# Optimization experiments

Measured on AMD Instinct MI355X. Metric: run time of the kernel, lower is better.

## Reference

```python
import jax, jax.numpy as jnp
import numpy as np

B, T, N, F = 8, 24, 207, 16
H = 64            # hidden_dim
DH = 16           # dims_hyper[-1] / node-embedding out
DA = 4 * F        # temporal attention dim_out
DS = 64           # ss_gal gcn out dim (last_ss_gal_dim)
GDEP = 2
ALPHA, BETA, GAMMA = 0.05, 0.95, 0.95
TA = 2.0


def _lin(x, w, b=None):
    y = x @ w
    return y if b is None else y + b


def gcn_hyper(x, A, W, b):
    # x: [B,N,C], A: [N,N] static. h <- a*x + g * einsum('nvc,vw->nwc', h, A)
    h = x
    outs = [h]
    for _ in range(GDEP):
        h = ALPHA * x + GAMMA * jnp.einsum('bvc,vw->bwc', h, A)
        outs.append(h)
    return _lin(jnp.concatenate(outs, axis=-1), W, b)


def gcn_gru(x, A_dyn, A_sta, W, b):
    # x: [B,N,C], A_dyn: [B,N,N], A_sta: [N,N]
    h = x
    outs = [h]
    for _ in range(GDEP):
        h = (ALPHA * x
             + BETA * jnp.einsum('bvw,bvc->bwc', A_dyn, h)     # bmm(A^T, h)
             + GAMMA * jnp.einsum('bvc,vw->bwc', h, A_sta))
        outs.append(h)
    return _lin(jnp.concatenate(outs, axis=-1), W, b)


def gcn_ssgal(x, A, W, b):
    # x: [B*,N,C], A: [B*,N,N]
    h = x
    outs = [h]
    for _ in range(GDEP):
        h = ALPHA * x + GAMMA * jnp.einsum('bvw,bvc->bwc', A, h)
        outs.append(h)
    return _lin(jnp.concatenate(outs, axis=-1), W, b)


def setup_inputs() -> dict:
    key = jax.random.key(0)
    ks = jax.random.split(key, 32)
    i = iter(range(32))
    w = lambda *s: (0.02 * jax.random.normal(ks[next(i)], s, dtype=jnp.float32))
    inp = {
        'input_sequence': jax.random.normal(ks[next(i)], (B, T, N, F), dtype=jnp.float32),
        'static_adj': jax.random.uniform(ks[next(i)], (N, N), dtype=jnp.float32),
        # hyper graph generators: mlp in = (GDEP+1)*H -> DH
        'src_gen_w': w((GDEP + 1) * H, DH), 'src_gen_b': w(DH),
        'tgt_gen_w': w((GDEP + 1) * H, DH), 'tgt_gen_b': w(DH),
        # node embeddings: F -> DH
        'src_emb_w': w(F, DH), 'src_emb_b': w(DH),
        'tgt_emb_w': w(F, DH), 'tgt_emb_b': w(DH),
        # GRU gate GCNs: mlp in = (GDEP+1)*(F+H) -> H
        'gru_z_w': w((GDEP + 1) * (F + H), H), 'gru_z_b': w(H),
        'gru_r_w': w((GDEP + 1) * (F + H), H), 'gru_r_b': w(H),
        'gru_c_w': w((GDEP + 1) * (F + H), H), 'gru_c_b': w(H),
        # temporal attention: F -> DA, score DA -> 1
        'attn_q_w': w(F, DA),
        'attn_k_w': w(F, DA), 'attn_k_b': w(DA),
        'attn_s_w': w(DA, 1),
        # ss_gal spatial gcn: (GDEP+1)*F -> DS
        'sgcn_w': w((GDEP + 1) * F, DS), 'sgcn_b': w(DS),
        # predictors
        'short_w': w(DS, F), 'short_b': w(F),
        'long_w': w(H, F), 'long_b': w(F),
        'fus_w': w(DS + H, F), 'fus_b': w(F),
    }
    return inp


def _forward(input_sequence, static_adj,
             src_gen_w, src_gen_b, tgt_gen_w, tgt_gen_b,
             src_emb_w, src_emb_b, tgt_emb_w, tgt_emb_b,
             gru_z_w, gru_z_b, gru_r_w, gru_r_b, gru_c_w, gru_c_b,
             attn_q_w, attn_k_w, attn_k_b, attn_s_w,
             sgcn_w, sgcn_b,
             short_w, short_b, long_w, long_b, fus_w, fus_b):
    batch, steps, nodes = input_sequence.shape[0], input_sequence.shape[1], input_sequence.shape[2]
    eye = jnp.eye(nodes, dtype=input_sequence.dtype)

    def cell(x_t, h):
        # x_t: [B,N,F], h: [B,N,H]
        src_ctx = gcn_hyper(h, static_adj, src_gen_w, src_gen_b)   # [B,N,DH]
        tgt_ctx = gcn_hyper(h, static_adj, tgt_gen_w, tgt_gen_b)
        s = jnp.tanh(TA * _lin(x_t, src_emb_w, src_emb_b) * src_ctx)
        t = jnp.tanh(TA * _lin(x_t, tgt_emb_w, tgt_emb_b) * tgt_ctx)
        asym = jnp.einsum('bnc,bmc->bnm', s, t) - jnp.einsum('bnc,bmc->bnm', t, s)
        adj = jax.nn.relu(jnp.tanh(TA * asym)) + eye
        adj = adj / (adj.sum(axis=-1, keepdims=True) + 1e-8)
        gi = jnp.concatenate([x_t, h], axis=-1)
        z = jax.nn.sigmoid(gcn_gru(gi, adj, static_adj, gru_z_w, gru_z_b))
        r = jax.nn.sigmoid(gcn_gru(gi, adj, static_adj, gru_r_w, gru_r_b))
        ri = jnp.concatenate([x_t, r * h], axis=-1)
        c = jnp.tanh(gcn_gru(ri, adj, static_adj, gru_c_w, gru_c_b))
        return z * h + (1.0 - z) * c

    h = jnp.zeros((batch, nodes, H), dtype=input_sequence.dtype)
    for t_step in range(0, max(1, steps - 4), 4):
        h = cell(input_sequence[:, t_step], h)

    # ss_gal branch on the last 4 steps
    recent = input_sequence[:, -4:]            # [B,4,N,F]
    target = input_sequence[:, -1]             # [B,N,F]
    # temporal attention
    q = target @ attn_q_w                      # [B,N,DA]
    k = recent @ attn_k_w + attn_k_b           # [B,4,N,DA]
    scores = jnp.tanh(q[:, None, :, None, :] + k[:, :, None, :, :])  # [B,4,N,N,DA]
    scores = jnp.squeeze(scores @ attn_s_w, axis=-1)                  # [B,4,N,N]
    attn = jax.nn.softmax(scores, axis=-1)
    dyn_adj = static_adj[None] + attn.reshape(-1, nodes, nodes)       # [B*4,N,N]
    rh = recent.reshape(-1, nodes, recent.shape[-1])                  # [B*4,N,F]
    rh = gcn_ssgal(rh, dyn_adj, sgcn_w, sgcn_b)                       # [B*4,N,DS]
    rh = jax.nn.relu(rh.reshape(batch, -1, nodes, rh.shape[-1]))      # [B,4,N,DS]
    target = jnp.sum(rh, axis=1)                                       # [B,N,DS]

    short = _lin(target, short_w, short_b)      # [B,N,F]
    h = cell(short, h)                          # final GRU step on short-term prediction
    long = _lin(h, long_w, long_b)              # [B,N,F]
    fused = _lin(jnp.concatenate([target, h], axis=-1), fus_w, fus_b)  # [B,N,F]
    return jnp.stack([short, long, fused], axis=0)  # [3,B,N,F]


def reference(input_sequence, static_adj,
              src_gen_w, src_gen_b, tgt_gen_w, tgt_gen_b,
              src_emb_w, src_emb_b, tgt_emb_w, tgt_emb_b,
              gru_z_w, gru_z_b, gru_r_w, gru_r_b, gru_c_w, gru_c_b,
              attn_q_w, attn_k_w, attn_k_b, attn_s_w,
              sgcn_w, sgcn_b,
              short_w, short_b, long_w, long_b, fus_w, fus_b):
    return _forward(input_sequence, static_adj,
                    src_gen_w, src_gen_b, tgt_gen_w, tgt_gen_b,
                    src_emb_w, src_emb_b, tgt_emb_w, tgt_emb_b,
                    gru_z_w, gru_z_b, gru_r_w, gru_r_b, gru_c_w, gru_c_b,
                    attn_q_w, attn_k_w, attn_k_b, attn_s_w,
                    sgcn_w, sgcn_b,
                    short_w, short_b, long_w, long_b, fus_w, fus_b)
```

## Files before the change

kernel.cpp:

```cpp
#include <hip/hip_runtime.h>


constexpr int B = 8, T = 24, N = 207, F = 16, H = 64, DH = 16;
constexpr int PS = 208;
constexpr float ALPHA = 0.05f, BETA = 0.95f, GAMMA = 0.95f, TA = 2.0f;
constexpr int NF = N * F;
constexpr int BNF = B * N * F;

__device__ __forceinline__ float tanh_fast(float x) { float e = __expf(2.f * x); return 1.f - 2.f / (e + 1.f); }
__device__ __forceinline__ float sigm(float x) { return 1.f / (1.f + __expf(-x)); }
__device__ __forceinline__ float tanh_pnc(float x) {
    float x2 = x * x;
    float p = x * (27.f + x2);
    float q = 27.f + 9.f * x2;
    return p * __builtin_amdgcn_rcpf(q);
}

__global__ __launch_bounds__(256) void k_build_Ts(const float* __restrict__ adj, float* __restrict__ Ts) {
    int i = blockIdx.x * 256 + threadIdx.x;
    if (i >= N * N) return;
    int w = i / N, v = i % N;
    Ts[(size_t)w * PS + v] = adj[v * N + w];
}

__global__ __launch_bounds__(256) void k_mm_sq(const float* __restrict__ Ain, float* __restrict__ Aout) {
    const float* A = Ain;
    float* O = Aout;
    int w0 = blockIdx.x * 32, v0b = blockIdx.y * 32;
    int tid = threadIdx.x;
    __shared__ float sA[2][32][33], sB[2][32][33];
    float acc[4] = {0, 0, 0, 0};
    int i0 = tid >> 5, j = tid & 31;
    int r = tid >> 3, c4 = (tid & 7) * 4;
    float4 av, bv;
    auto loadT = [&](int u0) {
        av = make_float4(0, 0, 0, 0); bv = make_float4(0, 0, 0, 0);
        int w = w0 + r, u = u0 + r;
        if (w < N) av = *(const float4*)&A[(size_t)w * PS + u0 + c4];
        if (u < N) bv = *(const float4*)&A[(size_t)u * PS + v0b + c4];
    };
    loadT(0);
    int cur = 0;
    for (int t = 0; t < 7; t++) {
        __syncthreads();
        sA[cur][r][c4] = av.x; sA[cur][r][c4 + 1] = av.y; sA[cur][r][c4 + 2] = av.z; sA[cur][r][c4 + 3] = av.w;
        sB[cur][r][c4] = bv.x; sB[cur][r][c4 + 1] = bv.y; sB[cur][r][c4 + 2] = bv.z; sB[cur][r][c4 + 3] = bv.w;
        if (t < 6) loadT((t + 1) * 32);
        __syncthreads();
#pragma unroll 8
        for (int u_ = 0; u_ < 32; u_++) {
            float bvv = sB[cur][u_][j];
#pragma unroll
            for (int k = 0; k < 4; k++) acc[k] += sA[cur][i0 + k * 8][u_] * bvv;
        }
        cur ^= 1;
    }
#pragma unroll
    for (int k = 0; k < 4; k++) {
        int w = w0 + i0 + k * 8, v = v0b + j;
        if (w < N && v < N) O[(size_t)w * PS + v] = acc[k];
    }
}

__global__ __launch_bounds__(256) void k_cell_a(
    const float* __restrict__ h, const float* __restrict__ Ts, const float* __restrict__ A2,
    const float* __restrict__ xseq, int tsel, const float* __restrict__ xbuf,
    const float* __restrict__ Wsrc, const float* __restrict__ bsrc,
    const float* __restrict__ Wtgt, const float* __restrict__ btgt,
    const float* __restrict__ Wes, const float* __restrict__ bes,
    const float* __restrict__ Wet, const float* __restrict__ bet,
    float* __restrict__ s_out, float* __restrict__ t_out, float* __restrict__ catg) {
    int b = blockIdx.y, w0 = blockIdx.x * 16, lane = blockIdx.z;
    int tid = threadIdx.x, ty = tid >> 4, tx = tid & 15;
    __shared__ float sTs[2][16][33], sA2[2][16][33];
    __shared__ float sH[2][32][64];
    __shared__ float cat[16][193];
    __shared__ float sW[192][16];
    __shared__ float sX[16][16], sWe[16][16];
    float au[4] = {0, 0, 0, 0}, aw[4] = {0, 0, 0, 0};
    const float* hb = h + b * N * H;
    const float* xp = (tsel >= 0) ? (xseq + ((size_t)(b * T + tsel)) * NF) : (xbuf + (size_t)b * NF);
    int pidx = tid & 127;
    int pr = pidx >> 3, pc4 = (pidx & 7) * 4;
    float4 t4;
    float4 h4[2];
    int hr[2], hc[2];
#pragma unroll
    for (int k = 0; k < 2; k++) { int l4 = tid + k * 256; hr[k] = l4 >> 4; hc[k] = (l4 & 15) * 4; }
    auto loadT = [&](int v0) {
        t4 = make_float4(0, 0, 0, 0);
        const float* src = (tid < 128) ? Ts : A2;
        int w = w0 + pr;
        if (w < N) t4 = *(const float4*)&src[(size_t)w * PS + v0 + pc4];
#pragma unroll
        for (int k = 0; k < 2; k++) {
            float4 hv = make_float4(0, 0, 0, 0);
            int v = v0 + hr[k];
            if (v < N) hv = *(const float4*)&hb[(size_t)v * H + hc[k]];
            h4[k] = hv;
        }
    };
    loadT(0);
    int cur = 0;
    for (int t = 0; t < 7; t++) {
        __syncthreads();
        {
            float (*dst)[33] = (tid < 128) ? sTs[cur] : sA2[cur];
            dst[pr][pc4] = t4.x; dst[pr][pc4 + 1] = t4.y; dst[pr][pc4 + 2] = t4.z; dst[pr][pc4 + 3] = t4.w;
        }
#pragma unroll
        for (int k = 0; k < 2; k++) *(float4*)&sH[cur][hr[k]][hc[k]] = h4[k];
        if (t < 6) loadT((t + 1) * 32);
        __syncthreads();
#pragma unroll 8
        for (int v = 0; v < 32; v++) {
            float pu = sTs[cur][ty][v], pw = sA2[cur][ty][v];
#pragma unroll
            for (int j = 0; j < 4; j++) {
                float x = sH[cur][v][tx * 4 + j];
                au[j] += pu * x; aw[j] += pw * x;
            }
        }
        cur ^= 1;
    }
    int w = w0 + ty;
    bool valid = w < N;
    __syncthreads();
    if (valid) {
#pragma unroll
        for (int j = 0; j < 4; j++) {
            int c = tx * 4 + j;
            float hv = hb[(size_t)w * H + c];
            float u = au[j], w2 = aw[j];
            cat[ty][c] = hv;
            cat[ty][64 + c] = ALPHA * hv + GAMMA * u;
            cat[ty][128 + c] = ALPHA * hv + ALPHA * GAMMA * u + GAMMA * GAMMA * w2;
        }
    } else {
#pragma unroll
        for (int j = 0; j < 4; j++) {
            int c = tx * 4 + j;
            cat[ty][c] = 0; cat[ty][64 + c] = 0; cat[ty][128 + c] = 0;
        }
    }
    const float* Wg = lane ? Wtgt : Wsrc;
    const float* bg = lane ? btgt : bsrc;
    const float* We = lane ? Wet : Wes;
    const float* be = lane ? bet : bes;
    {
        float4 wv[3];
#pragma unroll
        for (int k = 0; k < 3; k++) wv[k] = *(const float4*)&Wg[(tid + k * 256) * 4];
        float4 xv = make_float4(0, 0, 0, 0), ev = make_float4(0, 0, 0, 0);
        int sr = 0, sc = 0;
        if (tid < 64) {
            sr = tid >> 2; sc = (tid & 3) * 4;
            int n = w0 + sr;
            if (n < N) xv = *(const float4*)&xp[(size_t)n * F + sc];
            ev = *(const float4*)&We[tid * 4];
        }
#pragma unroll
        for (int k = 0; k < 3; k++) {
            int l4 = tid + k * 256;
            int r = l4 >> 2, c4 = (l4 & 3) * 4;
            *(float4*)&sW[r][c4] = wv[k];
        }
        if (tid < 64) {
            *(float4*)&sX[sr][sc] = xv;
            *(float4*)&sWe[sr][sc] = ev;
        }
    }
    __syncthreads();
    if (lane == 0 && valid) {
#pragma unroll
        for (int j = 0; j < 5; j++) {
            int c = tx * 5 + j;
            float v = (c < 16) ? sX[ty][c] : hb[(size_t)w * H + (c - 16)];
            catg[((size_t)(b * N + w)) * 240 + c] = v;
        }
    }
    {
        float ctx = bg[tx];
#pragma unroll 8
        for (int c = 0; c < 192; c++) ctx += cat[ty][c] * sW[c][tx];
        float xe = be[tx];
#pragma unroll
        for (int f = 0; f < 16; f++) xe += sX[ty][f] * sWe[f][tx];
        if (valid) {
            float val = tanh_fast(TA * xe * ctx);
            if (lane == 0) s_out[(size_t)(b * N + w) * DH + tx] = val;
            else           t_out[(size_t)(b * N + w) * DH + tx] = val;
        }
    }
}

__global__ __launch_bounds__(256) void k_cell_bP(const float* __restrict__ s_in, const float* __restrict__ t_in,
                                                 const float* __restrict__ adj, float* __restrict__ P) {
    int b = blockIdx.y, v0 = blockIdx.x * 16;
    int tid = threadIdx.x, ty = tid >> 4, tx = tid & 15;
    __shared__ float sS[N][17], sT[N][17];
    for (int l4 = tid; l4 < 828; l4 += 256) {
        float4 sv = *(const float4*)&s_in[(size_t)b * N * 16 + l4 * 4];
        float4 tv = *(const float4*)&t_in[(size_t)b * N * 16 + l4 * 4];
        int r = l4 >> 2, c = (l4 & 3) * 4;
        sS[r][c] = sv.x; sS[r][c + 1] = sv.y; sS[r][c + 2] = sv.z; sS[r][c + 3] = sv.w;
        sT[r][c] = tv.x; sT[r][c + 1] = tv.y; sT[r][c + 2] = tv.z; sT[r][c + 3] = tv.w;
    }
    __syncthreads();
    int v = v0 + ty;
    bool valid = v < N;
    int vc = valid ? v : (N - 1);
    float sv[16], tv[16];
#pragma unroll
    for (int k = 0; k < 16; k++) { sv[k] = sS[vc][k]; tv[k] = sT[vc][k]; }
    float val[13];
    float rsum = 0.f;
#pragma unroll
    for (int idx = 0; idx < 13; idx++) {
        int w = tx + 16 * idx;
        float r = 0.f;
        if (w < N) {
            float a = 0.f;
#pragma unroll
            for (int k = 0; k < 16; k++) a += sv[k] * sT[w][k] - tv[k] * sS[w][k];
            r = tanh_fast(TA * a);
            r = r > 0.f ? r : 0.f;
            if (w == v) r += 1.f;
        }
        val[idx] = r;
        rsum += r;
    }
    float tot = rsum;
    for (int d = 8; d > 0; d >>= 1) tot += __shfl_down(tot, d, 16);
    tot = __shfl(tot, 0, 16);
    float rinv = BETA / (tot + 1e-8f);
    if (valid) {
        float* Pb = P + (size_t)b * PS * PS;
#pragma unroll
        for (int idx = 0; idx < 13; idx++) {
            int w = tx + 16 * idx;
            if (w < N) Pb[(size_t)w * PS + v] = val[idx] * rinv + GAMMA * adj[v * N + w];
        }
    }
}

__global__ __launch_bounds__(256) void k_prop1(const float* __restrict__ P, float* __restrict__ cat) {
    int b = blockIdx.y, w0 = blockIdx.x * 16, c0 = blockIdx.z * 16;
    int tid = threadIdx.x, ty = tid >> 4, tx = tid & 15;
    const float* Pb = P + (size_t)b * PS * PS;
    __shared__ float sP[2][16][33], sX[2][32][17];
    float a1 = 0.f;
    int pr = tid >> 4, pc = (tid & 15) * 2;
    int xr = tid >> 3, xc = (tid & 7) * 2;
    float2 pv, xv;
    auto loadT = [&](int v0) {
        pv = make_float2(0, 0); xv = make_float2(0, 0);
        int w = w0 + pr;
        if (w < N) pv = *(const float2*)&Pb[(size_t)w * PS + v0 + pc];
        int vv = v0 + xr;
        if (vv < N) xv = *(const float2*)&cat[((size_t)(b * N + vv)) * 240 + c0 + xc];
    };
    loadT(0);
    int cur = 0;
    for (int t = 0; t < 7; t++) {
        __syncthreads();
        sP[cur][pr][pc] = pv.x; sP[cur][pr][pc + 1] = pv.y;
        sX[cur][xr][xc] = xv.x; sX[cur][xr][xc + 1] = xv.y;
        if (t < 6) loadT((t + 1) * 32);
        __syncthreads();
#pragma unroll 8
        for (int v_ = 0; v_ < 32; v_++) a1 += sP[cur][ty][v_] * sX[cur][v_][tx];
        cur ^= 1;
    }
    int w = w0 + ty, c = c0 + tx;
    if (w < N) {
        size_t base = ((size_t)(b * N + w)) * 240;
        cat[base + 80 + c] = ALPHA * cat[base + c] + a1;
    }
}

__global__ __launch_bounds__(256) void k_gate(
    const float* __restrict__ cat, const float* __restrict__ P,
    const float* __restrict__ Wa, const float* __restrict__ ba,
    const float* __restrict__ Wb, const float* __restrict__ bb,
    int baseMode,
    const float* __restrict__ xseq, int tsel, const float* __restrict__ xbuf,
    float* __restrict__ zbuf, float* __restrict__ ricat,
    float* __restrict__ h,
    const float* __restrict__ target,
    const float* __restrict__ Wlong, const float* __restrict__ blong,
    const float* __restrict__ Wfus, const float* __restrict__ bfus,
    float* __restrict__ out) {
    int mode = baseMode + blockIdx.z;
    const float* W = (mode == 1) ? Wb : Wa;
    const float* bias = (mode == 1) ? bb : ba;
    int b = blockIdx.y, w0 = blockIdx.x * 16;
    int tid = threadIdx.x, ty = tid >> 4, tx = tid & 15;
    const float* Pb = P + (size_t)b * PS * PS;
    __shared__ float sC[16][241];
    __shared__ float sP[16][33];
    __shared__ float sX[32][81];
    __shared__ float sW[48][65];
    __shared__ float hrow[16][65], trow[16][65];
    for (int l4 = tid; l4 < 640; l4 += 256) {
        int r = l4 / 40, c4 = (l4 % 40) * 4;
        int w = w0 + r;
        float4 v4 = make_float4(0, 0, 0, 0);
        if (w < N) v4 = *(const float4*)&cat[((size_t)(b * N + w)) * 240 + c4];
        sC[r][c4] = v4.x; sC[r][c4 + 1] = v4.y; sC[r][c4 + 2] = v4.z; sC[r][c4 + 3] = v4.w;
    }
    float acc[5] = {0, 0, 0, 0, 0};
    int prr = tid >> 4, prc = (tid & 15) * 2;
    int xrow = tid & 31, xc0 = (tid >> 5) * 10;
    float2 pv;
    float2 xv[5];
    auto loadT = [&](int v0) {
        pv = make_float2(0, 0);
        int w = w0 + prr;
        if (w < N) pv = *(const float2*)&Pb[(size_t)w * PS + v0 + prc];
        int v = v0 + xrow;
#pragma unroll
        for (int k = 0; k < 5; k++) xv[k] = make_float2(0, 0);
        if (v < N) {
            const float* src = &cat[((size_t)(b * N + v)) * 240 + 80 + xc0];
#pragma unroll
            for (int k = 0; k < 5; k++) xv[k] = *(const float2*)&src[k * 2];
        }
    };
    loadT(0);
    for (int t = 0; t < 7; t++) {
        __syncthreads();
        sP[prr][prc] = pv.x; sP[prr][prc + 1] = pv.y;
#pragma unroll
        for (int k = 0; k < 5; k++) { sX[xrow][xc0 + 2 * k] = xv[k].x; sX[xrow][xc0 + 2 * k + 1] = xv[k].y; }
        if (t < 6) loadT((t + 1) * 32);
        __syncthreads();
#pragma unroll 8
        for (int v = 0; v < 32; v++) {
            float p = sP[ty][v];
#pragma unroll
            for (int j = 0; j < 5; j++) acc[j] += p * sX[v][tx * 5 + j];
        }
    }
#pragma unroll
    for (int j = 0; j < 5; j++) {
        int c = tx * 5 + j;
        sC[ty][160 + c] = ALPHA * sC[ty][c] + acc[j];
    }
    float4 wv[3];
#pragma unroll
    for (int k = 0; k < 3; k++) wv[k] = *(const float4*)&W[(tid + k * 256) * 4];
    float ga[4];
#pragma unroll
    for (int j = 0; j < 4; j++) ga[j] = bias[tx * 4 + j];
    for (int ch = 0; ch < 5; ch++) {
        __syncthreads();
#pragma unroll
        for (int k = 0; k < 3; k++) {
            int l4 = tid + k * 256;
            int r = l4 >> 4, cc = (l4 & 15) * 4;
            sW[r][cc] = wv[k].x; sW[r][cc + 1] = wv[k].y; sW[r][cc + 2] = wv[k].z; sW[r][cc + 3] = wv[k].w;
        }
        if (ch < 4) {
#pragma unroll
            for (int k = 0; k < 3; k++) wv[k] = *(const float4*)&W[(size_t)(ch + 1) * 3072 + (tid + k * 256) * 4];
        }
        __syncthreads();
        int c0 = ch * 48;
#pragma unroll 8
        for (int cc = 0; cc < 48; cc++) {
            float cv = sC[ty][c0 + cc];
#pragma unroll
            for (int j = 0; j < 4; j++) ga[j] += cv * sW[cc][tx * 4 + j];
        }
    }
    int w = w0 + ty;
    bool valid = w < N;
    if (mode == 0) {
        if (valid) {
#pragma unroll
            for (int j = 0; j < 4; j++) zbuf[((size_t)(b * N + w)) * 64 + tx * 4 + j] = sigm(ga[j]);
        }
    } else if (mode == 1) {
        if (valid) {
#pragma unroll
            for (int j = 0; j < 4; j++) {
                int o = tx * 4 + j;
                ricat[((size_t)(b * N + w)) * 240 + 16 + o] = sigm(ga[j]) * h[((size_t)(b * N + w)) * 64 + o];
            }
            if (tx < 4) {
                const float* xp = (tsel >= 0) ? (xseq + ((size_t)(b * T + tsel)) * NF) : (xbuf + (size_t)b * NF);
#pragma unroll
                for (int j = 0; j < 4; j++) {
                    int c = tx * 4 + j;
                    ricat[((size_t)(b * N + w)) * 240 + c] = xp[w * F + c];
                }
            }
        }
    } else {
#pragma unroll
        for (int j = 0; j < 4; j++) {
            int o = tx * 4 + j;
            float cval = tanh_fast(ga[j]);
            float zv = 0.f, hv = 0.f;
            if (valid) { zv = zbuf[((size_t)(b * N + w)) * 64 + o]; hv = h[((size_t)(b * N + w)) * 64 + o]; }
            float hn = zv * hv + (1.f - zv) * cval;
            if (valid) h[((size_t)(b * N + w)) * 64 + o] = hn;
            hrow[ty][o] = valid ? hn : 0.f;
        }
        if (mode == 3) {
            for (int l = tid; l < 1024; l += 256) {
                int i = l >> 6, o = l & 63;
                int ww = w0 + i;
                trow[i][o] = (ww < N) ? target[((size_t)(b * N + ww)) * 64 + o] : 0.f;
            }
            __syncthreads();
            float lg = blong[tx];
            float fs = bfus[tx];
            for (int o = 0; o < 64; o++) {
                lg += hrow[ty][o] * Wlong[o * 16 + tx];
                fs += trow[ty][o] * Wfus[o * 16 + tx] + hrow[ty][o] * Wfus[(64 + o) * 16 + tx];
            }
            if (valid) {
                out[((size_t)1 * B * N + b * N + w) * 16 + tx] = lg;
                out[((size_t)2 * B * N + b * N + w) * 16 + tx] = fs;
            }
        }
    }
}

__global__ __launch_bounds__(256) void k_attn2(const float* __restrict__ inp,
                                               const float* __restrict__ Wq, const float* __restrict__ Wk,
                                               const float* __restrict__ kb, const float* __restrict__ sw_,
                                               float* __restrict__ attnT, float* __restrict__ rsum) {
    int bt = blockIdx.z, b = bt >> 2, tau = bt & 3;
    int n0 = blockIdx.x * 32, m0 = blockIdx.y * 32;
    int tid = threadIdx.x, ti = tid >> 4, tj = tid & 15;
    __shared__ float sQ[32][65], sK[32][65];
    __shared__ float sWq[16][64], sWk[16][64];
    __shared__ float sXq[32][17], sXk[32][17];
    __shared__ float ssw[64], skb[64];
    const float* xq = inp + ((size_t)(b * T + (T - 1))) * NF;
    const float* xk = inp + ((size_t)(b * T + 20 + tau)) * NF;
    {
        float4 wq4 = *(const float4*)&Wq[tid * 4];
        float4 wk4 = *(const float4*)&Wk[tid * 4];
        *(float4*)&sWq[tid >> 4][(tid & 15) * 4] = wq4;
        *(float4*)&sWk[tid >> 4][(tid & 15) * 4] = wk4;
        if (tid < 64) { ssw[tid] = sw_[tid]; skb[tid] = kb[tid]; }
        int idx = tid & 127;
        int r = idx >> 2, c4 = (idx & 3) * 4;
        if (tid < 128) {
            float4 a = make_float4(0, 0, 0, 0);
            int n = n0 + r;
            if (n < N) a = *(const float4*)&xq[(size_t)n * F + c4];
            sXq[r][c4] = a.x; sXq[r][c4 + 1] = a.y; sXq[r][c4 + 2] = a.z; sXq[r][c4 + 3] = a.w;
        } else {
            float4 c = make_float4(0, 0, 0, 0);
            int m = m0 + r;
            if (m < N) c = *(const float4*)&xk[(size_t)m * F + c4];
            sXk[r][c4] = c.x; sXk[r][c4 + 1] = c.y; sXk[r][c4 + 2] = c.z; sXk[r][c4 + 3] = c.w;
        }
    }
    __syncthreads();
    {
        int r = tid >> 3, o0 = (tid & 7) * 8;
        float xr[16], xkr[16];
#pragma unroll
        for (int f = 0; f < 16; f++) { xr[f] = sXq[r][f]; xkr[f] = sXk[r][f]; }
#pragma unroll
        for (int j = 0; j < 8; j++) {
            int o = o0 + j;
            float aq = 0.f, ak = skb[o];
#pragma unroll
            for (int f = 0; f < 16; f++) { aq += xr[f] * sWq[f][o]; ak += xkr[f] * sWk[f][o]; }
            sQ[r][o] = aq; sK[r][o] = ak;
        }
    }
    __syncthreads();
    float s00 = 0.f, s01 = 0.f, s10 = 0.f, s11 = 0.f;
#pragma unroll 2
    for (int d = 0; d < 64; d++) {
        float w = ssw[d];
        float q1 = sQ[ti][d], q2 = sQ[ti + 16][d];
        float k1 = sK[tj][d], k2 = sK[tj + 16][d];
        s00 += tanh_pnc(q1 + k1) * w;
        s01 += tanh_pnc(q1 + k2) * w;
        s10 += tanh_pnc(q2 + k1) * w;
        s11 += tanh_pnc(q2 + k2) * w;
    }
    int n1 = n0 + ti, n2 = n0 + ti + 16, m1 = m0 + tj, m2 = m0 + tj + 16;
    bool vn1 = n1 < N, vn2 = n2 < N, vm1 = m1 < N, vm2 = m2 < N;
    float e00 = (vn1 && vm1) ? __expf(s00) : 0.f;
    float e01 = (vn1 && vm2) ? __expf(s01) : 0.f;
    float e10 = (vn2 && vm1) ? __expf(s10) : 0.f;
    float e11 = (vn2 && vm2) ? __expf(s11) : 0.f;
    float part1 = e00 + e01, part2 = e10 + e11;
    for (int d = 8; d > 0; d >>= 1) {
        part1 += __shfl_down(part1, d, 16);
        part2 += __shfl_down(part2, d, 16);
    }
    if (tj == 0) {
        if (vn1) atomicAdd(&rsum[bt * N + n1], part1);
        if (vn2) atomicAdd(&rsum[bt * N + n2], part2);
    }
    __syncthreads();
    float* tile = &sQ[0][0];
    tile[tj * 33 + ti] = e00;
    tile[(tj + 16) * 33 + ti] = e01;
    tile[tj * 33 + ti + 16] = e10;
    tile[(tj + 16) * 33 + ti + 16] = e11;
    __syncthreads();
    {
        int row = tid >> 3, c4 = (tid & 7) * 4;
        int m = m0 + row;
        if (m < N) {
            float4 v = make_float4(tile[row * 33 + c4], tile[row * 33 + c4 + 1],
                                   tile[row * 33 + c4 + 2], tile[row * 33 + c4 + 3]);
            *(float4*)&attnT[(size_t)bt * PS * PS + (size_t)m * PS + n0 + c4] = v;
        }
    }
}

__global__ __launch_bounds__(256) void k_prop_xr(const float* __restrict__ attnT, const float* __restrict__ rsum,
                                                 const float* __restrict__ Ts, const float* __restrict__ inp,
                                                 float* __restrict__ x1) {
    int bt = blockIdx.y, w0 = blockIdx.x * 16;
    int b = bt >> 2, tau = bt & 3;
    const float* xb = inp + ((size_t)(b * T + 20 + tau)) * NF;
    const float* PA = attnT + (size_t)bt * PS * PS;
    int tid = threadIdx.x, ty = tid >> 4, tx = tid & 15;
    __shared__ float sPA[2][16][33], sPT[2][16][33];
    __shared__ float sX[2][32][17], sXs[2][32][17];
    float accA = 0.f, accT = 0.f;
    int prr = tid >> 3, pcc = (tid & 7) * 4;
    int xrr = (tid - 128) >> 2, xcc = ((tid - 128) & 3) * 4;
    float4 pa, pt, xv;
    float rinv_;
    auto loadT = [&](int v0) {
        pa = make_float4(0, 0, 0, 0); pt = make_float4(0, 0, 0, 0); xv = make_float4(0, 0, 0, 0); rinv_ = 0.f;
        if (tid < 128) {
            int w = w0 + prr;
            if (w < N) {
                pa = *(const float4*)&PA[(size_t)w * PS + v0 + pcc];
                pt = *(const float4*)&Ts[(size_t)w * PS + v0 + pcc];
            }
        } else {
            int v = v0 + xrr;
            if (v < N) {
                xv = *(const float4*)&xb[(size_t)v * F + xcc];
                rinv_ = __builtin_amdgcn_rcpf(rsum[bt * N + v]);
            }
        }
    };
    loadT(0);
    int cur = 0;
    for (int t = 0; t < 7; t++) {
        __syncthreads();
        if (tid < 128) {
            sPA[cur][prr][pcc] = pa.x; sPA[cur][prr][pcc + 1] = pa.y; sPA[cur][prr][pcc + 2] = pa.z; sPA[cur][prr][pcc + 3] = pa.w;
            sPT[cur][prr][pcc] = pt.x; sPT[cur][prr][pcc + 1] = pt.y; sPT[cur][prr][pcc + 2] = pt.z; sPT[cur][prr][pcc + 3] = pt.w;
        } else {
            sX[cur][xrr][xcc] = xv.x; sX[cur][xrr][xcc + 1] = xv.y; sX[cur][xrr][xcc + 2] = xv.z; sX[cur][xrr][xcc + 3] = xv.w;
            sXs[cur][xrr][xcc] = xv.x * rinv_; sXs[cur][xrr][xcc + 1] = xv.y * rinv_;
            sXs[cur][xrr][xcc + 2] = xv.z * rinv_; sXs[cur][xrr][xcc + 3] = xv.w * rinv_;
        }
        if (t < 6) loadT((t + 1) * 32);
        __syncthreads();
#pragma unroll 8
        for (int v = 0; v < 32; v++) {
            accA += sPA[cur][ty][v] * sXs[cur][v][tx];
            accT += sPT[cur][ty][v] * sX[cur][v][tx];
        }
        cur ^= 1;
    }
    int w = w0 + ty;
    if (w < N) x1[((size_t)(bt * N + w)) * 16 + tx] = ALPHA * xb[w * F + tx] + GAMMA * (accA + accT);
}

__global__ __launch_bounds__(256) void k_sgc2(const float* __restrict__ attnT, const float* __restrict__ rsum,
                                              const float* __restrict__ Ts, const float* __restrict__ x1,
                                              const float* __restrict__ inp,
                                              const float* __restrict__ Ws, const float* __restrict__ bs,
                                              float* __restrict__ target) {
    int bt = blockIdx.y, b = bt >> 2, tau = bt & 3, w0 = blockIdx.x * 16;
    const float* xb = inp + ((size_t)(b * T + 20 + tau)) * NF;
    const float* PA = attnT + (size_t)bt * PS * PS;
    int tid = threadIdx.x, ty = tid >> 4, tx = tid & 15;
    __shared__ float sPA[2][16][33], sPT[2][16][33];
    __shared__ float sX[2][32][17], sXs[2][32][17];
    __shared__ float cat[16][48], sW[48][64];
    float accA = 0.f, accT = 0.f;
    int prr = tid >> 3, pcc = (tid & 7) * 4;
    int xrr = (tid - 128) >> 2, xcc = ((tid - 128) & 3) * 4;
    float4 pa, pt, xv;
    float rinv_;
    auto loadT = [&](int v0) {
        pa = make_float4(0, 0, 0, 0); pt = make_float4(0, 0, 0, 0); xv = make_float4(0, 0, 0, 0); rinv_ = 0.f;
        if (tid < 128) {
            int w = w0 + prr;
            if (w < N) {
                pa = *(const float4*)&PA[(size_t)w * PS + v0 + pcc];
                pt = *(const float4*)&Ts[(size_t)w * PS + v0 + pcc];
            }
        } else {
            int v = v0 + xrr;
            if (v < N) {
                xv = *(const float4*)&x1[((size_t)(bt * N + v)) * 16 + xcc];
                rinv_ = __builtin_amdgcn_rcpf(rsum[bt * N + v]);
            }
        }
    };
    loadT(0);
    int cur = 0;
    for (int t = 0; t < 7; t++) {
        __syncthreads();
        if (tid < 128) {
            sPA[cur][prr][pcc] = pa.x; sPA[cur][prr][pcc + 1] = pa.y; sPA[cur][prr][pcc + 2] = pa.z; sPA[cur][prr][pcc + 3] = pa.w;
            sPT[cur][prr][pcc] = pt.x; sPT[cur][prr][pcc + 1] = pt.y; sPT[cur][prr][pcc + 2] = pt.z; sPT[cur][prr][pcc + 3] = pt.w;
        } else {
            sX[cur][xrr][xcc] = xv.x; sX[cur][xrr][xcc + 1] = xv.y; sX[cur][xrr][xcc + 2] = xv.z; sX[cur][xrr][xcc + 3] = xv.w;
            sXs[cur][xrr][xcc] = xv.x * rinv_; sXs[cur][xrr][xcc + 1] = xv.y * rinv_;
            sXs[cur][xrr][xcc + 2] = xv.z * rinv_; sXs[cur][xrr][xcc + 3] = xv.w * rinv_;
        }
        if (t < 6) loadT((t + 1) * 32);
        __syncthreads();
#pragma unroll 8
        for (int v = 0; v < 32; v++) {
            accA += sPA[cur][ty][v] * sXs[cur][v][tx];
            accT += sPT[cur][ty][v] * sX[cur][v][tx];
        }
        cur ^= 1;
    }
    int w = w0 + ty;
    bool valid = w < N;
    __syncthreads();
    for (int l = tid; l < 512; l += 256) {
        int i = l >> 5, c = l & 31;
        int ww = w0 + i;
        float vv = 0;
        if (ww < N) {
            if (c < 16) vv = xb[ww * F + c];
            else vv = x1[((size_t)bt * N + ww) * 16 + (c - 16)];
        }
        cat[i][c] = vv;
    }
    {
        float x0 = valid ? xb[w * F + tx] : 0.f;
        cat[ty][32 + tx] = ALPHA * x0 + GAMMA * (accA + accT);
    }
    {
        float4 wv[3];
#pragma unroll
        for (int k = 0; k < 3; k++) wv[k] = *(const float4*)&Ws[(tid + k * 256) * 4];
#pragma unroll
        for (int k = 0; k < 3; k++) {
            int l4 = tid + k * 256;
            *(float4*)&sW[l4 >> 4][(l4 & 15) * 4] = wv[k];
        }
    }
    __syncthreads();
    float a[4];
#pragma unroll
    for (int j = 0; j < 4; j++) a[j] = bs[tx * 4 + j];
#pragma unroll 8
    for (int cc = 0; cc < 48; cc++) {
        float cv = cat[ty][cc];
#pragma unroll
        for (int j = 0; j < 4; j++) a[j] += cv * sW[cc][tx * 4 + j];
    }
    if (valid) {
#pragma unroll
        for (int j = 0; j < 4; j++) {
            float r = a[j] > 0.f ? a[j] : 0.f;
            atomicAdd(&target[(b * N + w) * 64 + tx * 4 + j], r);
        }
    }
}

__global__ __launch_bounds__(256) void k_short(const float* __restrict__ target,
                                               const float* __restrict__ Wsh, const float* __restrict__ bsh,
                                               float* __restrict__ out, float* __restrict__ xshort) {
    int b = blockIdx.y, n0 = blockIdx.x * 16;
    int tid = threadIdx.x, ty = tid >> 4, tx = tid & 15;
    __shared__ float trow[16][65], sW[64][16];
    {
        int r = tid >> 4, c4 = (tid & 15) * 4;
        int n = n0 + r;
        float4 tv = make_float4(0, 0, 0, 0);
        if (n < N) tv = *(const float4*)&target[((size_t)(b * N + n)) * 64 + c4];
        trow[r][c4] = tv.x; trow[r][c4 + 1] = tv.y; trow[r][c4 + 2] = tv.z; trow[r][c4 + 3] = tv.w;
        float4 wv = *(const float4*)&Wsh[tid * 4];
        *(float4*)&sW[tid >> 2][(tid & 3) * 4] = wv;
    }
    __syncthreads();
    float a = bsh[tx];
#pragma unroll 8
    for (int o = 0; o < 64; o++) a += trow[ty][o] * sW[o][tx];
    int n = n0 + ty;
    if (n < N) {
        out[((size_t)0 * B * N + b * N + n) * 16 + tx] = a;
        xshort[(b * N + n) * 16 + tx] = a;
    }
}

extern "C" void kernel_launch(void* const* d_in, const int* in_sizes, int n_in,
                              void* d_out, int out_size, void* d_ws, size_t ws_size,
                              hipStream_t stream) {
    const float* inp = (const float*)d_in[0];
    const float* adj = (const float*)d_in[1];
    const float* src_gen_w = (const float*)d_in[2];
    const float* src_gen_b = (const float*)d_in[3];
    const float* tgt_gen_w = (const float*)d_in[4];
    const float* tgt_gen_b = (const float*)d_in[5];
    const float* src_emb_w = (const float*)d_in[6];
    const float* src_emb_b = (const float*)d_in[7];
    const float* tgt_emb_w = (const float*)d_in[8];
    const float* tgt_emb_b = (const float*)d_in[9];
    const float* gru_z_w = (const float*)d_in[10];
    const float* gru_z_b = (const float*)d_in[11];
    const float* gru_r_w = (const float*)d_in[12];
    const float* gru_r_b = (const float*)d_in[13];
    const float* gru_c_w = (const float*)d_in[14];
    const float* gru_c_b = (const float*)d_in[15];
    const float* attn_q_w = (const float*)d_in[16];
    const float* attn_k_w = (const float*)d_in[17];
    const float* attn_k_b = (const float*)d_in[18];
    const float* attn_s_w = (const float*)d_in[19];
    const float* sgcn_w = (const float*)d_in[20];
    const float* sgcn_b = (const float*)d_in[21];
    const float* short_w = (const float*)d_in[22];
    const float* short_b = (const float*)d_in[23];
    const float* long_w = (const float*)d_in[24];
    const float* long_b = (const float*)d_in[25];
    const float* fus_w = (const float*)d_in[26];
    const float* fus_b = (const float*)d_in[27];
    float* out = (float*)d_out;

    float* ws = (float*)d_ws;
    size_t off = 0;
    auto A = [&](size_t n) { n = (n + 3) & ~(size_t)3; float* p = ws + off; off += n; return p; };
    float* Ts = A((size_t)PS * PS);
    float* A2 = A((size_t)PS * PS);
    float* sbuf = A((size_t)B * N * DH);
    float* tbuf = A((size_t)B * N * DH);
    float* P = A((size_t)B * PS * PS);
    float* catg = A((size_t)B * N * 240);
    float* catc = A((size_t)B * N * 240);
    float* zb = A((size_t)B * N * 64);
    float* attnT = A((size_t)32 * PS * PS);
    float* x1 = A((size_t)32 * NF);
    float* xshort = A(BNF);
    size_t zero_begin = off;
    float* h = A((size_t)B * N * H);
    float* target = A((size_t)B * N * 64);
    float* rsum = A((size_t)32 * N);
    size_t zero_end = off;
    (void)ws_size; (void)in_sizes; (void)n_in; (void)out_size;

    hipMemsetAsync(h, 0, (zero_end - zero_begin) * sizeof(float), stream);
    k_build_Ts<<<(N * N + 255) / 256, 256, 0, stream>>>(adj, Ts);
    k_mm_sq<<<dim3(7, 7), 256, 0, stream>>>(Ts, A2);

    auto run_cell = [&](int tsel, const float* xbuf, int finalFlag) {
        k_cell_a<<<dim3(13, B, 2), 256, 0, stream>>>(h, Ts, A2, inp, tsel, xbuf,
                                                     src_gen_w, src_gen_b, tgt_gen_w, tgt_gen_b,
                                                     src_emb_w, src_emb_b, tgt_emb_w, tgt_emb_b, sbuf, tbuf, catg);
        k_cell_bP<<<dim3(13, B), 256, 0, stream>>>(sbuf, tbuf, adj, P);
        k_prop1<<<dim3(13, B, 5), 256, 0, stream>>>(P, catg);
        k_gate<<<dim3(13, B, 2), 256, 0, stream>>>(catg, P, gru_z_w, gru_z_b, gru_r_w, gru_r_b, 0,
                                                   inp, tsel, xbuf, zb, catc, h,
                                                   nullptr, nullptr, nullptr, nullptr, nullptr, nullptr);
        k_prop1<<<dim3(13, B, 5), 256, 0, stream>>>(P, catc);
        k_gate<<<dim3(13, B, 1), 256, 0, stream>>>(catc, P, gru_c_w, gru_c_b, nullptr, nullptr, 2 + finalFlag,
                                                   nullptr, 0, nullptr, zb, nullptr, h,
                                                   target, long_w, long_b, fus_w, fus_b, out);
    };

    for (int t = 0; t < 20; t += 4) run_cell(t, nullptr, 0);

    k_attn2<<<dim3(7, 7, 32), 256, 0, stream>>>(inp, attn_q_w, attn_k_w, attn_k_b, attn_s_w, attnT, rsum);
    k_prop_xr<<<dim3(13, 32), 256, 0, stream>>>(attnT, rsum, Ts, inp, x1);
    k_sgc2<<<dim3(13, 32), 256, 0, stream>>>(attnT, rsum, Ts, x1, inp, sgcn_w, sgcn_b, target);
    k_short<<<dim3(13, B), 256, 0, stream>>>(target, short_w, short_b, out, xshort);

    run_cell(-1, xshort, 1);
}
```

Baseline: 645.6 us.

## Merge adjacency setup and temporal attention into one front-loaded kernel

Replaces the separate transpose, adjacency-squaring and attention-score kernels with a single launch whose blocks are split by index into three roles. A2 is now computed straight from adj instead of waiting on the transposed Ts. The attention computation, which depends only on the inputs, moves ahead of the recurrent GRU loop, so its blocks run alongside the setup work. This removes two launches and the Ts-to-A2 dependency, but the shared-memory footprint is sized for the largest role, which may lower occupancy for the small blocks.

```diff
diff --git a/kernel.cpp b/kernel.cpp
--- a/kernel.cpp
+++ b/kernel.cpp
@@ -16,49 +16,143 @@
     return p * __builtin_amdgcn_rcpf(q);
 }
 
-__global__ __launch_bounds__(256) void k_build_Ts(const float* __restrict__ adj, float* __restrict__ Ts) {
-    int i = blockIdx.x * 256 + threadIdx.x;
-    if (i >= N * N) return;
-    int w = i / N, v = i % N;
-    Ts[(size_t)w * PS + v] = adj[v * N + w];
-}
-
-__global__ __launch_bounds__(256) void k_mm_sq(const float* __restrict__ Ain, float* __restrict__ Aout) {
-    const float* A = Ain;
-    float* O = Aout;
-    int w0 = blockIdx.x * 32, v0b = blockIdx.y * 32;
-    int tid = threadIdx.x;
-    __shared__ float sA[2][32][33], sB[2][32][33];
-    float acc[4] = {0, 0, 0, 0};
-    int i0 = tid >> 5, j = tid & 31;
-    int r = tid >> 3, c4 = (tid & 7) * 4;
-    float4 av, bv;
-    auto loadT = [&](int u0) {
-        av = make_float4(0, 0, 0, 0); bv = make_float4(0, 0, 0, 0);
-        int w = w0 + r, u = u0 + r;
-        if (w < N) av = *(const float4*)&A[(size_t)w * PS + u0 + c4];
-        if (u < N) bv = *(const float4*)&A[(size_t)u * PS + v0b + c4];
-    };
-    loadT(0);
-    int cur = 0;
-    for (int t = 0; t < 7; t++) {
-        __syncthreads();
-        sA[cur][r][c4] = av.x; sA[cur][r][c4 + 1] = av.y; sA[cur][r][c4 + 2] = av.z; sA[cur][r][c4 + 3] = av.w;
-        sB[cur][r][c4] = bv.x; sB[cur][r][c4 + 1] = bv.y; sB[cur][r][c4 + 2] = bv.z; sB[cur][r][c4 + 3] = bv.w;
-        if (t < 6) loadT((t + 1) * 32);
-        __syncthreads();
-#pragma unroll 8
-        for (int u_ = 0; u_ < 32; u_++) {
-            float bvv = sB[cur][u_][j];
-#pragma unroll
-            for (int k = 0; k < 4; k++) acc[k] += sA[cur][i0 + k * 8][u_] * bvv;
-        }
-        cur ^= 1;
-    }
-#pragma unroll
-    for (int k = 0; k < 4; k++) {
-        int w = w0 + i0 + k * 8, v = v0b + j;
-        if (w < N && v < N) O[(size_t)w * PS + v] = acc[k];
+__global__ __launch_bounds__(256) void k_stage0(
+    const float* __restrict__ adj, const float* __restrict__ inp,
+    const float* __restrict__ Wq, const float* __restrict__ Wk,
+    const float* __restrict__ kb, const float* __restrict__ sw_,
+    float* __restrict__ Ts, float* __restrict__ A2,
+    float* __restrict__ attnT, float* __restrict__ rsum)
+{
+    __shared__ float smem[7424];
+    int bid = blockIdx.x, tid = threadIdx.x;
+    if (bid < 49) {
+        int vb = (bid % 7) * 32, wb = (bid / 7) * 32;
+        float* sA = smem;
+        float* sB = smem + 1056;
+        float acc[4] = {0, 0, 0, 0};
+        int i0 = tid >> 5, j = tid & 31;
+        for (int u0 = 0; u0 < N; u0 += 32) {
+            __syncthreads();
+            for (int l = tid; l < 1024; l += 256) {
+                int i = l >> 5, jj = l & 31;
+                int v = vb + i, u = u0 + jj;
+                sA[i * 33 + jj] = (v < N && u < N) ? adj[v * N + u] : 0.f;
+                int uu = u0 + i, w = wb + jj;
+                sB[i * 33 + jj] = (uu < N && w < N) ? adj[uu * N + w] : 0.f;
+            }
+            __syncthreads();
+#pragma unroll 8
+            for (int u = 0; u < 32; u++) {
+                float bv = sB[u * 33 + j];
+#pragma unroll
+                for (int k = 0; k < 4; k++) acc[k] += sA[(i0 + k * 8) * 33 + u] * bv;
+            }
+        }
+#pragma unroll
+        for (int k = 0; k < 4; k++) {
+            int v = vb + i0 + k * 8, w = wb + j;
+            if (v < N && w < N) A2[(size_t)w * PS + v] = acc[k];
+        }
+    } else if (bid < 217) {
+        int i = (bid - 49) * 256 + tid;
+        if (i < N * N) {
+            int w = i / N, v = i % N;
+            Ts[(size_t)w * PS + v] = adj[v * N + w];
+        }
+    } else {
+        int idx = bid - 217;
+        int bt = idx / 49, rem = idx % 49;
+        int n0 = (rem % 7) * 32, m0 = (rem / 7) * 32;
+        int b = bt >> 2, tau = bt & 3;
+        int ti = tid >> 4, tj = tid & 15;
+        float* sQ = smem;
+        float* sK = smem + 2080;
+        float* sWq = smem + 4160;
+        float* sWk = smem + 5184;
+        float* sXq = smem + 6208;
+        float* sXk = smem + 6752;
+        float* ssw = smem + 7296;
+        float* skb = smem + 7360;
+        const float* xq = inp + ((size_t)(b * T + (T - 1))) * NF;
+        const float* xk = inp + ((size_t)(b * T + 20 + tau)) * NF;
+        {
+            float4 wq4 = *(const float4*)&Wq[tid * 4];
+            float4 wk4 = *(const float4*)&Wk[tid * 4];
+            *(float4*)&sWq[(tid >> 4) * 64 + (tid & 15) * 4] = wq4;
+            *(float4*)&sWk[(tid >> 4) * 64 + (tid & 15) * 4] = wk4;
+            if (tid < 64) { ssw[tid] = sw_[tid]; skb[tid] = kb[tid]; }
+            int i2 = tid & 127;
+            int r = i2 >> 2, c4 = (i2 & 3) * 4;
+            if (tid < 128) {
+                float4 a = make_float4(0, 0, 0, 0);
+                int n = n0 + r;
+                if (n < N) a = *(const float4*)&xq[(size_t)n * F + c4];
+                sXq[r * 17 + c4] = a.x; sXq[r * 17 + c4 + 1] = a.y; sXq[r * 17 + c4 + 2] = a.z; sXq[r * 17 + c4 + 3] = a.w;
+            } else {
+                float4 c = make_float4(0, 0, 0, 0);
+                int m = m0 + r;
+                if (m < N) c = *(const float4*)&xk[(size_t)m * F + c4];
+                sXk[r * 17 + c4] = c.x; sXk[r * 17 + c4 + 1] = c.y; sXk[r * 17 + c4 + 2] = c.z; sXk[r * 17 + c4 + 3] = c.w;
+            }
+        }
+        __syncthreads();
+        {
+            int r = tid >> 3, o0 = (tid & 7) * 8;
+            float xr[16], xkr[16];
+#pragma unroll
+            for (int f = 0; f < 16; f++) { xr[f] = sXq[r * 17 + f]; xkr[f] = sXk[r * 17 + f]; }
+#pragma unroll
+            for (int j = 0; j < 8; j++) {
+                int o = o0 + j;
+                float aq = 0.f, ak = skb[o];
+#pragma unroll
+                for (int f = 0; f < 16; f++) { aq += xr[f] * sWq[f * 64 + o]; ak += xkr[f] * sWk[f * 64 + o]; }
+                sQ[r * 65 + o] = aq; sK[r * 65 + o] = ak;
+            }
+        }
+        __syncthreads();
+        float s00 = 0.f, s01 = 0.f, s10 = 0.f, s11 = 0.f;
+#pragma unroll 2
+        for (int d = 0; d < 64; d++) {
+            float w = ssw[d];
+            float q1 = sQ[ti * 65 + d], q2 = sQ[(ti + 16) * 65 + d];
+            float k1 = sK[tj * 65 + d], k2 = sK[(tj + 16) * 65 + d];
+            s00 += tanh_pnc(q1 + k1) * w;
+            s01 += tanh_pnc(q1 + k2) * w;
+            s10 += tanh_pnc(q2 + k1) * w;
+            s11 += tanh_pnc(q2 + k2) * w;
+        }
+        int n1 = n0 + ti, n2 = n0 + ti + 16, m1 = m0 + tj, m2 = m0 + tj + 16;
+        bool vn1 = n1 < N, vn2 = n2 < N, vm1 = m1 < N, vm2 = m2 < N;
+        float e00 = (vn1 && vm1) ? __expf(s00) : 0.f;
+        float e01 = (vn1 && vm2) ? __expf(s01) : 0.f;
+        float e10 = (vn2 && vm1) ? __expf(s10) : 0.f;
+        float e11 = (vn2 && vm2) ? __expf(s11) : 0.f;
+        float part1 = e00 + e01, part2 = e10 + e11;
+        for (int d = 8; d > 0; d >>= 1) {
+            part1 += __shfl_down(part1, d, 16);
+            part2 += __shfl_down(part2, d, 16);
+        }
+        if (tj == 0) {
+            if (vn1) atomicAdd(&rsum[bt * N + n1], part1);
+            if (vn2) atomicAdd(&rsum[bt * N + n2], part2);
+        }
+        __syncthreads();
+        float* tile = sQ;
+        tile[tj * 33 + ti] = e00;
+        tile[(tj + 16) * 33 + ti] = e01;
+        tile[tj * 33 + ti + 16] = e10;
+        tile[(tj + 16) * 33 + ti + 16] = e11;
+        __syncthreads();
+        {
+            int row = tid >> 3, c4 = (tid & 7) * 4;
+            int m = m0 + row;
+            if (m < N) {
+                float4 v = make_float4(tile[row * 33 + c4], tile[row * 33 + c4 + 1],
+                                       tile[row * 33 + c4 + 2], tile[row * 33 + c4 + 3]);
+                *(float4*)&attnT[(size_t)bt * PS * PS + (size_t)m * PS + n0 + c4] = v;
+            }
+        }
     }
 }
 
@@ -425,99 +519,6 @@
                 out[((size_t)1 * B * N + b * N + w) * 16 + tx] = lg;
                 out[((size_t)2 * B * N + b * N + w) * 16 + tx] = fs;
             }
-        }
-    }
-}
-
-__global__ __launch_bounds__(256) void k_attn2(const float* __restrict__ inp,
-                                               const float* __restrict__ Wq, const float* __restrict__ Wk,
-                                               const float* __restrict__ kb, const float* __restrict__ sw_,
-                                               float* __restrict__ attnT, float* __restrict__ rsum) {
-    int bt = blockIdx.z, b = bt >> 2, tau = bt & 3;
-    int n0 = blockIdx.x * 32, m0 = blockIdx.y * 32;
-    int tid = threadIdx.x, ti = tid >> 4, tj = tid & 15;
-    __shared__ float sQ[32][65], sK[32][65];
-    __shared__ float sWq[16][64], sWk[16][64];
-    __shared__ float sXq[32][17], sXk[32][17];
-    __shared__ float ssw[64], skb[64];
-    const float* xq = inp + ((size_t)(b * T + (T - 1))) * NF;
-    const float* xk = inp + ((size_t)(b * T + 20 + tau)) * NF;
-    {
-        float4 wq4 = *(const float4*)&Wq[tid * 4];
-        float4 wk4 = *(const float4*)&Wk[tid * 4];
-        *(float4*)&sWq[tid >> 4][(tid & 15) * 4] = wq4;
-        *(float4*)&sWk[tid >> 4][(tid & 15) * 4] = wk4;
-        if (tid < 64) { ssw[tid] = sw_[tid]; skb[tid] = kb[tid]; }
-        int idx = tid & 127;
-        int r = idx >> 2, c4 = (idx & 3) * 4;
-        if (tid < 128) {
-            float4 a = make_float4(0, 0, 0, 0);
-            int n = n0 + r;
-            if (n < N) a = *(const float4*)&xq[(size_t)n * F + c4];
-            sXq[r][c4] = a.x; sXq[r][c4 + 1] = a.y; sXq[r][c4 + 2] = a.z; sXq[r][c4 + 3] = a.w;
-        } else {
-            float4 c = make_float4(0, 0, 0, 0);
-            int m = m0 + r;
-            if (m < N) c = *(const float4*)&xk[(size_t)m * F + c4];
-            sXk[r][c4] = c.x; sXk[r][c4 + 1] = c.y; sXk[r][c4 + 2] = c.z; sXk[r][c4 + 3] = c.w;
-        }
-    }
-    __syncthreads();
-    {
-        int r = tid >> 3, o0 = (tid & 7) * 8;
-        float xr[16], xkr[16];
-#pragma unroll
-        for (int f = 0; f < 16; f++) { xr[f] = sXq[r][f]; xkr[f] = sXk[r][f]; }
-#pragma unroll
-        for (int j = 0; j < 8; j++) {
-            int o = o0 + j;
-            float aq = 0.f, ak = skb[o];
-#pragma unroll
-            for (int f = 0; f < 16; f++) { aq += xr[f] * sWq[f][o]; ak += xkr[f] * sWk[f][o]; }
-            sQ[r][o] = aq; sK[r][o] = ak;
-        }
-    }
-    __syncthreads();
-    float s00 = 0.f, s01 = 0.f, s10 = 0.f, s11 = 0.f;
-#pragma unroll 2
-    for (int d = 0; d < 64; d++) {
-        float w = ssw[d];
-        float q1 = sQ[ti][d], q2 = sQ[ti + 16][d];
-        float k1 = sK[tj][d], k2 = sK[tj + 16][d];
-        s00 += tanh_pnc(q1 + k1) * w;
-        s01 += tanh_pnc(q1 + k2) * w;
-        s10 += tanh_pnc(q2 + k1) * w;
-        s11 += tanh_pnc(q2 + k2) * w;
-    }
-    int n1 = n0 + ti, n2 = n0 + ti + 16, m1 = m0 + tj, m2 = m0 + tj + 16;
-    bool vn1 = n1 < N, vn2 = n2 < N, vm1 = m1 < N, vm2 = m2 < N;
-    float e00 = (vn1 && vm1) ? __expf(s00) : 0.f;
-    float e01 = (vn1 && vm2) ? __expf(s01) : 0.f;
-    float e10 = (vn2 && vm1) ? __expf(s10) : 0.f;
-    float e11 = (vn2 && vm2) ? __expf(s11) : 0.f;
-    float part1 = e00 + e01, part2 = e10 + e11;
-    for (int d = 8; d > 0; d >>= 1) {
-        part1 += __shfl_down(part1, d, 16);
-        part2 += __shfl_down(part2, d, 16);
-    }
-    if (tj == 0) {
-        if (vn1) atomicAdd(&rsum[bt * N + n1], part1);
-        if (vn2) atomicAdd(&rsum[bt * N + n2], part2);
-    }
-    __syncthreads();
-    float* tile = &sQ[0][0];
-    tile[tj * 33 + ti] = e00;
-    tile[(tj + 16) * 33 + ti] = e01;
-    tile[tj * 33 + ti + 16] = e10;
-    tile[(tj + 16) * 33 + ti + 16] = e11;
-    __syncthreads();
-    {
-        int row = tid >> 3, c4 = (tid & 7) * 4;
-        int m = m0 + row;
-        if (m < N) {
-            float4 v = make_float4(tile[row * 33 + c4], tile[row * 33 + c4 + 1],
-                                   tile[row * 33 + c4 + 2], tile[row * 33 + c4 + 3]);
-            *(float4*)&attnT[(size_t)bt * PS * PS + (size_t)m * PS + n0 + c4] = v;
         }
     }
 }
@@ -759,8 +760,7 @@
     (void)ws_size; (void)in_sizes; (void)n_in; (void)out_size;
 
     hipMemsetAsync(h, 0, (zero_end - zero_begin) * sizeof(float), stream);
-    k_build_Ts<<<(N * N + 255) / 256, 256, 0, stream>>>(adj, Ts);
-    k_mm_sq<<<dim3(7, 7), 256, 0, stream>>>(Ts, A2);
+    k_stage0<<<1785, 256, 0, stream>>>(adj, inp, attn_q_w, attn_k_w, attn_k_b, attn_s_w, Ts, A2, attnT, rsum);
 
     auto run_cell = [&](int tsel, const float* xbuf, int finalFlag) {
         k_cell_a<<<dim3(13, B, 2), 256, 0, stream>>>(h, Ts, A2, inp, tsel, xbuf,
@@ -779,7 +779,6 @@
 
     for (int t = 0; t < 20; t += 4) run_cell(t, nullptr, 0);
 
-    k_attn2<<<dim3(7, 7, 32), 256, 0, stream>>>(inp, attn_q_w, attn_k_w, attn_k_b, attn_s_w, attnT, rsum);
     k_prop_xr<<<dim3(13, 32), 256, 0, stream>>>(attnT, rsum, Ts, inp, x1);
     k_sgc2<<<dim3(13, 32), 256, 0, stream>>>(attnT, rsum, Ts, x1, inp, sgcn_w, sgcn_b, target);
     k_short<<<dim3(13, B), 256, 0, stream>>>(target, short_w, short_b, out, xshort);
```

Measured after the change: 630.3 us. 1.02x faster.
